# Kernel tuning notes

Hardware: AMD Instinct MI355X
Metric: run time of the kernel (lower is better)

Reference implementation:

```python
import jax, jax.numpy as jnp
import numpy as np

B, S, D, H, L = 64, 512, 1024, 1024, 2


def setup_inputs() -> dict:
    key = jax.random.key(0)
    ks = jax.random.split(key, 12)
    x = jax.random.normal(ks[0], (B, S, D), dtype=jnp.float32)
    lengths = jax.random.randint(ks[1], (B,), 1, S + 1)
    lengths = lengths.at[0].set(S)  # ensure max len == S (matches torch trim)
    x_mask = (jnp.arange(S)[None, :] < lengths[:, None]).astype(jnp.float32)
    h0 = jax.random.normal(ks[2], (L, B, H), dtype=jnp.float32)
    sc = 1.0 / np.sqrt(H)
    p = {}
    p['Wih0'] = jax.random.uniform(ks[3], (3 * H, D), jnp.float32, -sc, sc)
    p['Whh0'] = jax.random.uniform(ks[4], (3 * H, H), jnp.float32, -sc, sc)
    p['bih0'] = jax.random.uniform(ks[5], (3 * H,), jnp.float32, -sc, sc)
    p['bhh0'] = jax.random.uniform(ks[6], (3 * H,), jnp.float32, -sc, sc)
    p['Wih1'] = jax.random.uniform(ks[7], (3 * H, H), jnp.float32, -sc, sc)
    p['Whh1'] = jax.random.uniform(ks[8], (3 * H, H), jnp.float32, -sc, sc)
    p['bih1'] = jax.random.uniform(ks[9], (3 * H,), jnp.float32, -sc, sc)
    p['bhh1'] = jax.random.uniform(ks[10], (3 * H,), jnp.float32, -sc, sc)
    return dict(x=x, x_mask=x_mask, h0=h0, **p)


def _gru_cell(xt, h, Wih, Whh, bih, bhh):
    # PyTorch gate order: r, z, n
    gi = xt @ Wih.T + bih          # [B, 3H]
    gh = h @ Whh.T + bhh           # [B, 3H]
    ir, iz, inn = jnp.split(gi, 3, axis=-1)
    hr, hz, hn = jnp.split(gh, 3, axis=-1)
    r = jax.nn.sigmoid(ir + hr)
    z = jax.nn.sigmoid(iz + hz)
    n = jnp.tanh(inn + r * hn)
    return (1.0 - z) * n + z * h


def reference(x, x_mask, h0, Wih0, Whh0, bih0, bhh0, Wih1, Whh1, bih1, bhh1):
    params = [(Wih0, Whh0, bih0, bhh0), (Wih1, Whh1, bih1, bhh1)]
    xs = jnp.swapaxes(x, 0, 1)        # [S, B, D]
    ms = x_mask.T                     # [S, B]

    def step(h, inp):
        xt, mt = inp                  # [B, D], [B]
        gate = (mt > 0.5)[:, None]    # packed seq: skip padded steps
        layer_in = xt
        new_hs = []
        for l, (Wih, Whh, bih, bhh) in enumerate(params):
            hl = h[l]
            hl_new = jnp.where(gate, _gru_cell(layer_in, hl, Wih, Whh, bih, bhh), hl)
            new_hs.append(hl_new)
            layer_in = hl_new
        h_new = jnp.stack(new_hs)
        return h_new, new_hs[-1] * mt[:, None]  # masked top-layer output

    h_final, outs = jax.lax.scan(step, h0, (xs, ms))
    output_pad = jnp.swapaxes(outs, 0, 1)        # [B, S, H]
    hidden = jnp.swapaxes(h_final, 0, 1)         # [B, L, H]
    return jnp.concatenate([output_pad, hidden], axis=1).mean(axis=1, keepdims=True)
```

## Files before the change

### kernel.cpp

```cpp
#include <hip/hip_runtime.h>
#include <hip/hip_fp16.h>

#define BB 64
#define SS 512
#define DD 1024
#define HH 1024
#define TICKS 515
#define NBLK 128

typedef _Float16 f16;
typedef unsigned long long u64;
typedef __attribute__((ext_vector_type(8))) _Float16 f16x8;
typedef __attribute__((ext_vector_type(4))) _Float16 f16x4;
typedef __attribute__((ext_vector_type(4))) float f32x4;

struct GruWS {
  unsigned cnt[4 * 8 * 64];
  f16 gi0[4][3 * HH][BB];
  f16 gi1[4][3 * HH][BB];
  f16 h0b[4][BB][HH];
  f16 h1b[4][BB][HH];
};

__device__ __forceinline__ f16x8 ld_sys_16B(const void* p) {
  f16x8 r;
  asm volatile("global_load_dwordx4 %0, %1, off sc0 sc1" : "=v"(r) : "v"(p) : "memory");
  return r;
}
__device__ __forceinline__ void st_mall_16B(void* p, f16x8 v) {
  union { f16x8 v; u64 q[2]; } u; u.v = v;
  asm volatile("global_atomic_swap_x2 %0, %1, off sc1" :: "v"((u64*)p), "v"(u.q[0]) : "memory");
  asm volatile("global_atomic_swap_x2 %0, %1, off sc1" :: "v"((u64*)p + 1), "v"(u.q[1]) : "memory");
}
__device__ __forceinline__ void st_mall_8B(void* p, u64 q) {
  asm volatile("global_atomic_swap_x2 %0, %1, off sc1" :: "v"((u64*)p), "v"(q) : "memory");
}
__device__ __forceinline__ void drain_vm() {
  asm volatile("s_waitcnt vmcnt(0)" ::: "memory");
  __builtin_amdgcn_sched_barrier(0);
}
__device__ __forceinline__ f16x4 ld_sys_f16x4(const f16* p) {
  u64 q = __hip_atomic_load((const u64*)p, __ATOMIC_RELAXED, __HIP_MEMORY_SCOPE_SYSTEM);
  union { u64 q; f16x4 v; } u; u.q = q; return u.v;
}
__device__ __forceinline__ float ld_sys_f16s(const f16* p) {
  unsigned short s = __hip_atomic_load((const unsigned short*)p, __ATOMIC_RELAXED, __HIP_MEMORY_SCOPE_SYSTEM);
  union { unsigned short s; f16 h; } u; u.s = s; return (float)u.h;
}

__device__ __forceinline__ void wait_done(unsigned* cnt, int role, int tick) {
  if (tick < 0) return;
  unsigned* c = &cnt[(role * 8 + (tick & 7)) * 64];
  const unsigned tgt = 32u * ((unsigned)tick / 8u + 1u);
  while (__hip_atomic_load(c, __ATOMIC_RELAXED, __HIP_MEMORY_SCOPE_SYSTEM) < tgt)
    __builtin_amdgcn_s_sleep(2);
  asm volatile("" ::: "memory");
}

__global__ void gru_init(const float* __restrict__ h0, GruWS* __restrict__ ws) {
  int i = blockIdx.x * 256 + threadIdx.x;
  int j = i * 4;
  if (j < 2 * BB * HH) {
    union { f16 h[4]; u64 q; } u;
#pragma unroll
    for (int k = 0; k < 4; ++k) u.h[k] = (f16)h0[j + k];
    if (j < BB * HH) st_mall_8B(&ws->h0b[3][0][j], u.q);
    else             st_mall_8B(&ws->h1b[3][0][j - BB * HH], u.q);
  }
  if (i < 4 * 8) {
    __hip_atomic_store(&ws->cnt[i * 64], 0u, __ATOMIC_RELAXED, __HIP_MEMORY_SCOPE_SYSTEM);
  }
}

__device__ __forceinline__ void mma_pass(const f16x8 areg[8][4], const f16x8* bnt,
                                         float* red, int lane, int wave, f32x4 acc[3]) {
  f32x4 pacc[4][3];
#pragma unroll
  for (int m = 0; m < 4; ++m)
#pragma unroll
    for (int g = 0; g < 3; ++g) pacc[m][g] = (f32x4){0.f, 0.f, 0.f, 0.f};
#pragma unroll
  for (int kk = 0; kk < 8; ++kk)
#pragma unroll
    for (int m = 0; m < 4; ++m)
#pragma unroll
      for (int g = 0; g < 3; ++g)
        pacc[m][g] = __builtin_amdgcn_mfma_f32_16x16x32_f16(areg[kk][m], bnt[g * 8 + kk], pacc[m][g], 0, 0, 0);
#pragma unroll
  for (int m = 0; m < 4; ++m)
    if (m != wave)
#pragma unroll
      for (int g = 0; g < 3; ++g)
#pragma unroll
        for (int r = 0; r < 4; ++r)
          red[(((wave * 4 + m) * 3 + g) * 4 + r) * 64 + lane] = pacc[m][g][r];
  __syncthreads();
#pragma unroll
  for (int g = 0; g < 3; ++g) {
    f32x4 a = pacc[wave][g];
#pragma unroll
    for (int sw = 0; sw < 4; ++sw)
      if (sw != wave)
#pragma unroll
        for (int r = 0; r < 4; ++r)
          a[r] += red[(((sw * 4 + wave) * 3 + g) * 4 + r) * 64 + lane];
    acc[g] = a;
  }
}

__global__ __launch_bounds__(256, 1) void gru_main(
    const float* __restrict__ x, const float* __restrict__ xmask,
    const float* __restrict__ h0in,
    const float* __restrict__ Wih0, const float* __restrict__ Whh0,
    const float* __restrict__ bih0, const float* __restrict__ bhh0,
    const float* __restrict__ Wih1, const float* __restrict__ Whh1,
    const float* __restrict__ bih1, const float* __restrict__ bhh1,
    float* __restrict__ out, GruWS* __restrict__ ws) {
  __shared__ __align__(16) char ldsbuf[49152];
  float* red = (float*)ldsbuf;

  const int bid = blockIdx.x;
  const int grp = bid >> 5;
  const int gidx = bid & 31;
  const int base = gidx * 32;
  const int tid = threadIdx.x;
  const int lane = tid & 63;
  const int wave = tid >> 6;
  const int l15 = lane & 15;
  const int kgrp = lane >> 4;
  const int b0 = wave * 16 + kgrp * 4;
  const int kbase0 = wave * 256 + kgrp * 8;
  unsigned* cnt = ws->cnt;

  const float* Wsrc = (grp == 0) ? Wih0 : (grp == 1) ? Whh0 : (grp == 2) ? Wih1 : Whh1;
  f16x8 breg[2][3][8];
#pragma unroll
  for (int nt = 0; nt < 2; ++nt)
#pragma unroll
    for (int g = 0; g < 3; ++g)
#pragma unroll
      for (int kk = 0; kk < 8; ++kk) {
        const float* p = Wsrc + (long)(g * HH + base + nt * 16 + l15) * DD + kbase0 + kk * 32;
        float4 v0 = *(const float4*)p;
        float4 v1 = *(const float4*)(p + 4);
        f16x8 t;
        t[0] = (f16)v0.x; t[1] = (f16)v0.y; t[2] = (f16)v0.z; t[3] = (f16)v0.w;
        t[4] = (f16)v1.x; t[5] = (f16)v1.y; t[6] = (f16)v1.z; t[7] = (f16)v1.w;
        breg[nt][g][kk] = t;
      }

  if (grp == 0 || grp == 2) {
    const int layer = (grp == 2);
    const float* bih = layer ? bih1 : bih0;
    const float* bhh = layer ? bhh1 : bhh0;
    float bias[2][3];
#pragma unroll
    for (int nt = 0; nt < 2; ++nt)
#pragma unroll
      for (int g = 0; g < 3; ++g) {
        int colg = base + nt * 16 + l15;
        bias[nt][g] = bih[g * HH + colg] + (g < 2 ? bhh[g * HH + colg] : 0.0f);
      }

    for (int t = 0; t < TICKS; ++t) {
      const int s = t - (layer ? 2 : 0);
      const bool active = (s >= 0 && s < SS);
      if (active && tid < 2) {
        int role, tk;
        if (!layer) { role = 1; tk = (tid == 0) ? t - 3 : -1; }
        else        { role = (tid == 0) ? 1 : 3;
                      tk   = (tid == 0) ? t - 1 : t - 3; }
        wait_done(cnt, role, tk);
      }
      __syncthreads();
      if (active) {
        f16x8 areg[8][4];
        if (!layer) {
#pragma unroll
          for (int kk = 0; kk < 8; ++kk)
#pragma unroll
            for (int m = 0; m < 4; ++m) {
              const float* p = x + (long)(m * 16 + l15) * (SS * DD) + (long)s * DD + kbase0 + kk * 32;
              float4 v0 = *(const float4*)p;
              float4 v1 = *(const float4*)(p + 4);
              f16x8 a;
              a[0] = (f16)v0.x; a[1] = (f16)v0.y; a[2] = (f16)v0.z; a[3] = (f16)v0.w;
              a[4] = (f16)v1.x; a[5] = (f16)v1.y; a[6] = (f16)v1.z; a[7] = (f16)v1.w;
              areg[kk][m] = a;
            }
        } else {
          const f16* A = &ws->h0b[s & 3][0][0];
#pragma unroll
          for (int kk = 0; kk < 8; ++kk)
#pragma unroll
            for (int m = 0; m < 4; ++m)
              areg[kk][m] = ld_sys_16B(A + (long)(m * 16 + l15) * HH + kbase0 + kk * 32);
          drain_vm();
        }
        f32x4 accs[2][3];
        mma_pass(areg, &breg[0][0][0], red, lane, wave, accs[0]);
        __syncthreads();
        mma_pass(areg, &breg[1][0][0], red, lane, wave, accs[1]);
        __syncthreads();

        f16* gt = (f16*)ldsbuf;
#pragma unroll
        for (int nt = 0; nt < 2; ++nt)
#pragma unroll
          for (int g = 0; g < 3; ++g) {
            f16x4 o;
#pragma unroll
            for (int r = 0; r < 4; ++r) o[r] = (f16)(accs[nt][g][r] + bias[nt][g]);
            *(f16x4*)(gt + (g * 32 + nt * 16 + l15) * 64 + b0) = o;
          }
        __syncthreads();
        f16* gib = layer ? &ws->gi1[s & 3][0][0] : &ws->gi0[s & 3][0][0];
#pragma unroll
        for (int rnd = 0; rnd < 3; ++rnd) {
          int idx = rnd * 256 + tid;
          int row = idx >> 3, ch = idx & 7;
          int g = row >> 5, c = row & 31;
          f16x8 v = *(const f16x8*)(gt + row * 64 + ch * 8);
          st_mall_16B(gib + (long)(g * HH + base + c) * BB + ch * 8, v);
        }
      }
      asm volatile("s_waitcnt vmcnt(0)" ::: "memory");
      __syncthreads();
      if (tid == 0)
        __hip_atomic_fetch_add(&cnt[(grp * 8 + (t & 7)) * 64], 1u,
                               __ATOMIC_RELAXED, __HIP_MEMORY_SCOPE_SYSTEM);
    }
  } else {
    const int layer = (grp == 3);
    const float* bhh = layer ? bhh1 : bhh0;
    float bhn[2], hold[2][4], osum[2][4];
#pragma unroll
    for (int nt = 0; nt < 2; ++nt) {
      bhn[nt] = bhh[2 * HH + base + nt * 16 + l15];
#pragma unroll
      for (int r = 0; r < 4; ++r) {
        hold[nt][r] = h0in[(long)layer * BB * HH + (long)(b0 + r) * HH + base + nt * 16 + l15];
        osum[nt][r] = 0.f;
      }
    }

    for (int t = 0; t < TICKS; ++t) {
      const int s = t - (layer ? 3 : 1);
      const bool active = (s >= 0 && s < SS);
      if (active && tid < 3) {
        int role, tk;
        if (!layer) {
          role = (tid == 0) ? 0 : (tid == 1) ? 1 : 2;
          tk   = (tid == 2) ? t - 3 : t - 1;
        } else {
          role = (tid == 0) ? 2 : 3;
          tk   = (tid < 2) ? t - 1 : -1;
        }
        wait_done(cnt, role, tk);
      }
      __syncthreads();
      if (active) {
        const f16* hprev = layer ? &ws->h1b[(s - 1) & 3][0][0] : &ws->h0b[(s - 1) & 3][0][0];
        const f16* gib = layer ? &ws->gi1[s & 3][0][0] : &ws->gi0[s & 3][0][0];
        f16x8 areg[8][4];
#pragma unroll
        for (int kk = 0; kk < 8; ++kk)
#pragma unroll
          for (int m = 0; m < 4; ++m)
            areg[kk][m] = ld_sys_16B(hprev + (long)(m * 16 + l15) * HH + kbase0 + kk * 32);
        f16x4 gfr[2][3];
#pragma unroll
        for (int nt = 0; nt < 2; ++nt)
#pragma unroll
          for (int g = 0; g < 3; ++g)
            gfr[nt][g] = ld_sys_f16x4(gib + (long)(g * HH + base + nt * 16 + l15) * BB + b0);
        float mv[4];
#pragma unroll
        for (int r = 0; r < 4; ++r) mv[r] = xmask[(long)(b0 + r) * SS + s];
        drain_vm();

        f32x4 accs[2][3];
        mma_pass(areg, &breg[0][0][0], red, lane, wave, accs[0]);
        __syncthreads();
        mma_pass(areg, &breg[1][0][0], red, lane, wave, accs[1]);
        __syncthreads();

        f16* htile = (f16*)ldsbuf;
#pragma unroll
        for (int nt = 0; nt < 2; ++nt)
#pragma unroll
          for (int r = 0; r < 4; ++r) {
            float pr = accs[nt][0][r] + (float)gfr[nt][0][r];
            float pz = accs[nt][1][r] + (float)gfr[nt][1][r];
            float ph = accs[nt][2][r] + bhn[nt];
            float rr = 1.0f / (1.0f + __expf(-pr));
            float zz = 1.0f / (1.0f + __expf(-pz));
            float nn = tanhf((float)gfr[nt][2][r] + rr * ph);
            float upd = hold[nt][r] + (1.0f - zz) * (nn - hold[nt][r]);
            if (mv[r] > 0.5f) {
              hold[nt][r] = upd;
              if (layer) osum[nt][r] += upd;
            }
            htile[(b0 + r) * 32 + nt * 16 + l15] = (f16)hold[nt][r];
          }
        __syncthreads();
        f16* hout = layer ? &ws->h1b[s & 3][0][0] : &ws->h0b[s & 3][0][0];
        {
          int b = tid >> 2, ch = tid & 3;
          f16x8 v = *(const f16x8*)(htile + b * 32 + ch * 8);
          st_mall_16B(hout + (long)b * HH + base + ch * 8, v);
        }
        if (s == SS - 1 && layer) {
#pragma unroll
          for (int nt = 0; nt < 2; ++nt)
#pragma unroll
            for (int r = 0; r < 4; ++r) {
              int colg = base + nt * 16 + l15;
              float h0f = ld_sys_f16s(&ws->h0b[3][b0 + r][colg]);
              out[(long)(b0 + r) * HH + colg] =
                  (osum[nt][r] + hold[nt][r] + h0f) * (1.0f / 514.0f);
            }
        }
      }
      asm volatile("s_waitcnt vmcnt(0)" ::: "memory");
      __syncthreads();
      if (tid == 0)
        __hip_atomic_fetch_add(&cnt[(grp * 8 + (t & 7)) * 64], 1u,
                               __ATOMIC_RELAXED, __HIP_MEMORY_SCOPE_SYSTEM);
    }
  }
}

extern "C" void kernel_launch(void* const* d_in, const int* in_sizes, int n_in,
                              void* d_out, int out_size, void* d_ws, size_t ws_size,
                              hipStream_t stream) {
  const float* x = (const float*)d_in[0];
  const float* xmask = (const float*)d_in[1];
  const float* h0 = (const float*)d_in[2];
  const float* Wih0 = (const float*)d_in[3];
  const float* Whh0 = (const float*)d_in[4];
  const float* bih0 = (const float*)d_in[5];
  const float* bhh0 = (const float*)d_in[6];
  const float* Wih1 = (const float*)d_in[7];
  const float* Whh1 = (const float*)d_in[8];
  const float* bih1 = (const float*)d_in[9];
  const float* bhh1 = (const float*)d_in[10];
  float* out = (float*)d_out;
  GruWS* ws = (GruWS*)d_ws;

  hipLaunchKernelGGL(gru_init, dim3(128), dim3(256), 0, stream, h0, ws);
  hipLaunchKernelGGL(gru_main, dim3(NBLK), dim3(256), 0, stream,
                     x, xmask, h0, Wih0, Whh0, bih0, bhh0,
                     Wih1, Whh1, bih1, bhh1, out, ws);
}
```

Measured before the change: 10.10 ms.

## Replace shared atomic counters with per-block tick flags polled wave-wide

Cross-block synchronization moves from atomic fetch-add counters, one per role and tick slot, to per-block monotonically increasing tick flags written with an atomic swap. A whole wave polls all 32 producer flags in parallel and checks them with a wave vote, and the different dependencies are waited on by different waves at the same time. This removes contention from 32 blocks incrementing the same counter and shortens the polling loop. The gi stores also change from two 8-byte atomic swaps to a single 16-byte store with system-coherence bits, which cuts the number of store instructions but depends on the drain before the flag write for visibility.

```diff
diff --git a/kernel.cpp b/kernel.cpp
--- a/kernel.cpp
+++ b/kernel.cpp
@@ -15,7 +15,7 @@
 typedef __attribute__((ext_vector_type(4))) float f32x4;
 
 struct GruWS {
-  unsigned cnt[4 * 8 * 64];
+  unsigned sig[4 * 32 * 16];
   f16 gi0[4][3 * HH][BB];
   f16 gi1[4][3 * HH][BB];
   f16 h0b[4][BB][HH];
@@ -27,6 +27,9 @@
   asm volatile("global_load_dwordx4 %0, %1, off sc0 sc1" : "=v"(r) : "v"(p) : "memory");
   return r;
 }
+__device__ __forceinline__ void st_sys_16B(void* p, f16x8 v) {
+  asm volatile("global_store_dwordx4 %0, %1, off sc0 sc1" :: "v"(p), "v"(v) : "memory");
+}
 __device__ __forceinline__ void st_mall_16B(void* p, f16x8 v) {
   union { f16x8 v; u64 q[2]; } u; u.v = v;
   asm volatile("global_atomic_swap_x2 %0, %1, off sc1" :: "v"((u64*)p), "v"(u.q[0]) : "memory");
@@ -35,6 +38,9 @@
 __device__ __forceinline__ void st_mall_8B(void* p, u64 q) {
   asm volatile("global_atomic_swap_x2 %0, %1, off sc1" :: "v"((u64*)p), "v"(q) : "memory");
 }
+__device__ __forceinline__ void sig_swap(unsigned* p, unsigned v) {
+  asm volatile("global_atomic_swap %0, %1, off sc1" :: "v"(p), "v"(v) : "memory");
+}
 __device__ __forceinline__ void drain_vm() {
   asm volatile("s_waitcnt vmcnt(0)" ::: "memory");
   __builtin_amdgcn_sched_barrier(0);
@@ -48,12 +54,17 @@
   union { unsigned short s; f16 h; } u; u.s = s; return (float)u.h;
 }
 
-__device__ __forceinline__ void wait_done(unsigned* cnt, int role, int tick) {
+__device__ __forceinline__ void wait_all(const unsigned* sigrole, int tick, int lane) {
   if (tick < 0) return;
-  unsigned* c = &cnt[(role * 8 + (tick & 7)) * 64];
-  const unsigned tgt = 32u * ((unsigned)tick / 8u + 1u);
-  while (__hip_atomic_load(c, __ATOMIC_RELAXED, __HIP_MEMORY_SCOPE_SYSTEM) < tgt)
-    __builtin_amdgcn_s_sleep(2);
+  const unsigned tgt = (unsigned)tick + 1u;
+  const unsigned* p = sigrole + (lane & 31) * 16;
+  for (;;) {
+    unsigned v;
+    asm volatile("global_load_dword %0, %1, off sc0 sc1" : "=v"(v) : "v"(p));
+    asm volatile("s_waitcnt vmcnt(0)" ::: "memory");
+    if (__all(v >= tgt)) break;
+    __builtin_amdgcn_s_sleep(1);
+  }
   asm volatile("" ::: "memory");
 }
 
@@ -67,8 +78,8 @@
     if (j < BB * HH) st_mall_8B(&ws->h0b[3][0][j], u.q);
     else             st_mall_8B(&ws->h1b[3][0][j - BB * HH], u.q);
   }
-  if (i < 4 * 8) {
-    __hip_atomic_store(&ws->cnt[i * 64], 0u, __ATOMIC_RELAXED, __HIP_MEMORY_SCOPE_SYSTEM);
+  if (i < 4 * 32) {
+    __hip_atomic_store(&ws->sig[i * 16], 0u, __ATOMIC_RELAXED, __HIP_MEMORY_SCOPE_SYSTEM);
   }
 }
 
@@ -130,7 +141,8 @@
   const int kgrp = lane >> 4;
   const int b0 = wave * 16 + kgrp * 4;
   const int kbase0 = wave * 256 + kgrp * 8;
-  unsigned* cnt = ws->cnt;
+  unsigned* sig = ws->sig;
+  unsigned* mysig = &sig[(grp * 32 + gidx) * 16];
 
   const float* Wsrc = (grp == 0) ? Wih0 : (grp == 1) ? Whh0 : (grp == 2) ? Wih1 : Whh1;
   f16x8 breg[2][3][8];
@@ -165,12 +177,13 @@
     for (int t = 0; t < TICKS; ++t) {
       const int s = t - (layer ? 2 : 0);
       const bool active = (s >= 0 && s < SS);
-      if (active && tid < 2) {
-        int role, tk;
-        if (!layer) { role = 1; tk = (tid == 0) ? t - 3 : -1; }
-        else        { role = (tid == 0) ? 1 : 3;
-                      tk   = (tid == 0) ? t - 1 : t - 3; }
-        wait_done(cnt, role, tk);
+      if (active) {
+        if (!layer) {
+          if (wave == 0) wait_all(&sig[1 * 32 * 16], t - 3, lane);
+        } else {
+          if (wave == 0) wait_all(&sig[1 * 32 * 16], t - 1, lane);
+          if (wave == 1) wait_all(&sig[3 * 32 * 16], t - 3, lane);
+        }
       }
       __syncthreads();
       if (active) {
@@ -221,14 +234,12 @@
           int row = idx >> 3, ch = idx & 7;
           int g = row >> 5, c = row & 31;
           f16x8 v = *(const f16x8*)(gt + row * 64 + ch * 8);
-          st_mall_16B(gib + (long)(g * HH + base + c) * BB + ch * 8, v);
+          st_sys_16B(gib + (long)(g * HH + base + c) * BB + ch * 8, v);
         }
       }
       asm volatile("s_waitcnt vmcnt(0)" ::: "memory");
       __syncthreads();
-      if (tid == 0)
-        __hip_atomic_fetch_add(&cnt[(grp * 8 + (t & 7)) * 64], 1u,
-                               __ATOMIC_RELAXED, __HIP_MEMORY_SCOPE_SYSTEM);
+      if (tid == 0) sig_swap(mysig, (unsigned)(t + 1));
     }
   } else {
     const int layer = (grp == 3);
@@ -247,16 +258,15 @@
     for (int t = 0; t < TICKS; ++t) {
       const int s = t - (layer ? 3 : 1);
       const bool active = (s >= 0 && s < SS);
-      if (active && tid < 3) {
-        int role, tk;
+      if (active) {
         if (!layer) {
-          role = (tid == 0) ? 0 : (tid == 1) ? 1 : 2;
-          tk   = (tid == 2) ? t - 3 : t - 1;
+          if (wave == 0) wait_all(&sig[0 * 32 * 16], t - 1, lane);
+          if (wave == 1) wait_all(&sig[1 * 32 * 16], t - 1, lane);
+          if (wave == 2) wait_all(&sig[2 * 32 * 16], t - 3, lane);
         } else {
-          role = (tid == 0) ? 2 : 3;
-          tk   = (tid < 2) ? t - 1 : -1;
-        }
-        wait_done(cnt, role, tk);
+          if (wave == 0) wait_all(&sig[2 * 32 * 16], t - 1, lane);
+          if (wave == 1) wait_all(&sig[3 * 32 * 16], t - 1, lane);
+        }
       }
       __syncthreads();
       if (active) {
@@ -324,9 +334,7 @@
       }
       asm volatile("s_waitcnt vmcnt(0)" ::: "memory");
       __syncthreads();
-      if (tid == 0)
-        __hip_atomic_fetch_add(&cnt[(grp * 8 + (t & 7)) * 64], 1u,
-                               __ATOMIC_RELAXED, __HIP_MEMORY_SCOPE_SYSTEM);
+      if (tid == 0) sig_swap(mysig, (unsigned)(t + 1));
     }
   }
 }
```

Result: faster. 9.321 ms (-7.7%).
